# Kernel tuning notes

Hardware: AMD Instinct MI355X
Metric: run time of the kernel (lower is better)

## Reference

```python
import jax, jax.numpy as jnp
import numpy as np

B, S, D = 4, 2048, 768
H, DK, DV = 12, 64, 64
NEG = -1e9
EPS = 1e-5  # torch LayerNorm default


def setup_inputs() -> dict:
    key = jax.random.key(0)
    ks = jax.random.split(key, 12)
    s = 0.02
    return {
        "Q": jax.random.normal(ks[0], (B, S, D), jnp.float32),
        "K": jax.random.normal(ks[1], (B, S, D), jnp.float32),
        "V": jax.random.normal(ks[2], (B, S, D), jnp.float32),
        "attn_pad": jax.random.randint(ks[3], (B, S, S), 0, 2).astype(bool),
        # weights stored [in, out] (transpose of torch Linear layout)
        "Wq": jax.random.normal(ks[4], (D, H * DK), jnp.float32) * s,
        "bq": jnp.zeros((H * DK,), jnp.float32),
        "Wk": jax.random.normal(ks[5], (D, H * DK), jnp.float32) * s,
        "bk": jnp.zeros((H * DK,), jnp.float32),
        "Wv": jax.random.normal(ks[6], (D, H * DV), jnp.float32) * s,
        "bv": jnp.zeros((H * DV,), jnp.float32),
        "Wo": jax.random.normal(ks[7], (H * DV, D), jnp.float32) * s,
        "bo": jnp.zeros((D,), jnp.float32),
        "ln_g": jnp.ones((D,), jnp.float32),
        "ln_b": jnp.zeros((D,), jnp.float32),
    }


def reference(Q, K, V, attn_pad, Wq, bq, Wk, bk, Wv, bv, Wo, bo, ln_g, ln_b):
    residual = Q
    # projections -> [B, H, S, d]
    q = (Q @ Wq + bq).reshape(B, S, H, DK).transpose(0, 2, 1, 3)
    k = (K @ Wk + bk).reshape(B, S, H, DK).transpose(0, 2, 1, 3)
    v = (V @ Wv + bv).reshape(B, S, H, DV).transpose(0, 2, 1, 3)
    # scaled dot-product attention with pad masking
    scores = jnp.einsum("bhqd,bhkd->bhqk", q, k) / np.sqrt(DK).astype(np.float32)
    scores = jnp.where(attn_pad[:, None, :, :], NEG, scores)
    attn = jax.nn.softmax(scores, axis=-1)
    context = jnp.einsum("bhqk,bhkd->bhqd", attn, v)
    context = context.transpose(0, 2, 1, 3).reshape(B, S, H * DV)
    out = context @ Wo + bo + residual
    # LayerNorm over last dim
    mu = jnp.mean(out, axis=-1, keepdims=True)
    var = jnp.mean(jnp.square(out - mu), axis=-1, keepdims=True)
    out = (out - mu) * jax.lax.rsqrt(var + EPS) * ln_g + ln_b
    return out, attn
```

## Files before the change

### kernel.cpp

```cpp
#include <hip/hip_runtime.h>
#include <hip/hip_bf16.h>

#define BB 4
#define SS 2048
#define DD 768
#define HH 12
#define DKV 64
#define NEGBIG (-1e30f)

__global__ __launch_bounds__(256) void proj_gemm(
    const float* __restrict__ X, const float* __restrict__ W,
    const float* __restrict__ bias, float* __restrict__ outp)
{
  const int K = DD, N = DD;
  const int row0 = blockIdx.x * 64;
  const int h    = blockIdx.y;
  const int col0 = h << 6;
  const int tid = threadIdx.x;
  const int ty = tid >> 4, tx = tid & 15;

  __shared__ __align__(16) float As[16 * 64];
  __shared__ __align__(16) float Bs[16 * 64];

  float acc[4][4] = {};
  for (int k0 = 0; k0 < K; k0 += 16) {
    {
      int r = tid >> 2, c = (tid & 3) << 2;
      float4 a4 = *(const float4*)&X[(size_t)(row0 + r) * K + k0 + c];
      As[(c + 0) * 64 + r] = a4.x; As[(c + 1) * 64 + r] = a4.y;
      As[(c + 2) * 64 + r] = a4.z; As[(c + 3) * 64 + r] = a4.w;
    }
    {
      int r = tid >> 4, c = (tid & 15) << 2;
      *(float4*)&Bs[r * 64 + c] = *(const float4*)&W[(size_t)(k0 + r) * N + col0 + c];
    }
    __syncthreads();
#pragma unroll
    for (int kk = 0; kk < 16; ++kk) {
      float4 a4 = *(float4*)&As[kk * 64 + ty * 4];
      float4 b4 = *(float4*)&Bs[kk * 64 + tx * 4];
      float a[4] = {a4.x, a4.y, a4.z, a4.w};
      float b[4] = {b4.x, b4.y, b4.z, b4.w};
#pragma unroll
      for (int i = 0; i < 4; i++)
#pragma unroll
        for (int j = 0; j < 4; j++) acc[i][j] += a[i] * b[j];
    }
    __syncthreads();
  }
  float4 bv4 = *(const float4*)&bias[col0 + tx * 4];
#pragma unroll
  for (int i = 0; i < 4; i++) {
    int row = row0 + ty * 4 + i;
    int b = row >> 11, s = row & (SS - 1);
    float4 o;
    o.x = acc[i][0] + bv4.x; o.y = acc[i][1] + bv4.y;
    o.z = acc[i][2] + bv4.z; o.w = acc[i][3] + bv4.w;
    *(float4*)&outp[(((size_t)b * HH + h) * SS + s) * DKV + tx * 4] = o;
  }
}

__global__ __launch_bounds__(256) void outproj_gemm(
    const float* __restrict__ X, const float* __restrict__ W,
    const float* __restrict__ bias, const float* __restrict__ resid,
    float* __restrict__ outp)
{
  const int K = DD, N = DD;
  const int row0 = blockIdx.x * 64;
  const int col0 = blockIdx.y << 6;
  const int tid = threadIdx.x;
  const int ty = tid >> 4, tx = tid & 15;

  __shared__ __align__(16) float As[16 * 64];
  __shared__ __align__(16) float Bs[16 * 64];

  float acc[4][4] = {};
  for (int k0 = 0; k0 < K; k0 += 16) {
    {
      int r = tid >> 2, c = (tid & 3) << 2;
      float4 a4 = *(const float4*)&X[(size_t)(row0 + r) * K + k0 + c];
      As[(c + 0) * 64 + r] = a4.x; As[(c + 1) * 64 + r] = a4.y;
      As[(c + 2) * 64 + r] = a4.z; As[(c + 3) * 64 + r] = a4.w;
    }
    {
      int r = tid >> 4, c = (tid & 15) << 2;
      *(float4*)&Bs[r * 64 + c] = *(const float4*)&W[(size_t)(k0 + r) * N + col0 + c];
    }
    __syncthreads();
#pragma unroll
    for (int kk = 0; kk < 16; ++kk) {
      float4 a4 = *(float4*)&As[kk * 64 + ty * 4];
      float4 b4 = *(float4*)&Bs[kk * 64 + tx * 4];
      float a[4] = {a4.x, a4.y, a4.z, a4.w};
      float b[4] = {b4.x, b4.y, b4.z, b4.w};
#pragma unroll
      for (int i = 0; i < 4; i++)
#pragma unroll
        for (int j = 0; j < 4; j++) acc[i][j] += a[i] * b[j];
    }
    __syncthreads();
  }
  float4 bv4 = *(const float4*)&bias[col0 + tx * 4];
#pragma unroll
  for (int i = 0; i < 4; i++) {
    int row = row0 + ty * 4 + i;
    float4 r4 = *(const float4*)&resid[(size_t)row * DD + col0 + tx * 4];
    float4 o;
    o.x = acc[i][0] + bv4.x + r4.x; o.y = acc[i][1] + bv4.y + r4.y;
    o.z = acc[i][2] + bv4.z + r4.z; o.w = acc[i][3] + bv4.w + r4.w;
    *(float4*)&outp[(size_t)row * DD + col0 + tx * 4] = o;
  }
}

__global__ __launch_bounds__(256) void attn_kernel(
    const float* __restrict__ qh, const float* __restrict__ kh,
    const float* __restrict__ vh, const int* __restrict__ pad,
    float* __restrict__ attn, float* __restrict__ ctx)
{
  const int qt = blockIdx.x, h = blockIdx.y, b = blockIdx.z;
  const int tid = threadIdx.x;
  const int ty = tid >> 4, tx = tid & 15;

  const float* qbase = qh + (((size_t)b * HH + h) * SS + qt * 64) * DKV;
  const float* kbase = kh + (((size_t)b * HH + h) * SS) * DKV;
  const float* vbase = vh + (((size_t)b * HH + h) * SS) * DKV;

  __shared__ __align__(16) float QsT[64 * 64];
  __shared__ __align__(16) float KV[64 * 64];
  __shared__ __align__(16) float Sc[64 * 68];
  __shared__ float red[64 * 4];
  __shared__ float mrow[64], lrow[64], mnew_s[64];

  {
    int r = tid >> 2, cb = (tid & 3) << 4;
    const float* qr = qbase + (size_t)r * DKV;
#pragma unroll
    for (int q = 0; q < 4; q++) {
      float4 v = *(const float4*)(qr + cb + q * 4);
      QsT[(cb + q * 4 + 0) * 64 + r] = v.x; QsT[(cb + q * 4 + 1) * 64 + r] = v.y;
      QsT[(cb + q * 4 + 2) * 64 + r] = v.z; QsT[(cb + q * 4 + 3) * 64 + r] = v.w;
    }
  }
  if (tid < 64) { mrow[tid] = NEGBIG; lrow[tid] = 0.f; }
  __syncthreads();

  for (int kc = 0; kc < SS / 64; ++kc) {
    int kc0 = kc << 6;
    {
      int r = tid >> 2, cb = (tid & 3) << 4;
      const float* krow = kbase + (size_t)(kc0 + r) * DKV;
#pragma unroll
      for (int q = 0; q < 4; q++) {
        float4 v = *(const float4*)(krow + cb + q * 4);
        KV[(cb + q * 4 + 0) * 64 + r] = v.x; KV[(cb + q * 4 + 1) * 64 + r] = v.y;
        KV[(cb + q * 4 + 2) * 64 + r] = v.z; KV[(cb + q * 4 + 3) * 64 + r] = v.w;
      }
    }
    __syncthreads();
    float s[4][4] = {};
#pragma unroll 16
    for (int kk = 0; kk < 64; ++kk) {
      float4 a4 = *(float4*)&QsT[kk * 64 + ty * 4];
      float4 b4 = *(float4*)&KV[kk * 64 + tx * 4];
      float a[4] = {a4.x, a4.y, a4.z, a4.w};
      float bb[4] = {b4.x, b4.y, b4.z, b4.w};
#pragma unroll
      for (int i = 0; i < 4; i++)
#pragma unroll
        for (int j = 0; j < 4; j++) s[i][j] += a[i] * bb[j];
    }
#pragma unroll
    for (int i = 0; i < 4; i++) {
      int qglob = qt * 64 + ty * 4 + i;
      const int4 pm = *(const int4*)&pad[((size_t)b * SS + qglob) * SS + kc0 + tx * 4];
      float4 o;
      o.x = pm.x ? -1e9f : s[i][0] * 0.125f;
      o.y = pm.y ? -1e9f : s[i][1] * 0.125f;
      o.z = pm.z ? -1e9f : s[i][2] * 0.125f;
      o.w = pm.w ? -1e9f : s[i][3] * 0.125f;
      *(float4*)&Sc[(ty * 4 + i) * 68 + tx * 4] = o;
    }
    __syncthreads();
    {
      int r = tid >> 2, seg = tid & 3;
      const float* srow = &Sc[r * 68 + seg * 16];
      float mx = NEGBIG;
#pragma unroll
      for (int t = 0; t < 16; t++) mx = fmaxf(mx, srow[t]);
      red[r * 4 + seg] = mx;
      __syncthreads();
      if (seg == 0) {
        float cm = fmaxf(fmaxf(red[r * 4], red[r * 4 + 1]),
                         fmaxf(red[r * 4 + 2], red[r * 4 + 3]));
        mnew_s[r] = fmaxf(mrow[r], cm);
      }
      __syncthreads();
      float mn = mnew_s[r];
      float se = 0.f;
#pragma unroll
      for (int t = 0; t < 16; t++) se += __expf(srow[t] - mn);
      red[r * 4 + seg] = se;
      __syncthreads();
      if (seg == 0) {
        float ssum = red[r * 4] + red[r * 4 + 1] + red[r * 4 + 2] + red[r * 4 + 3];
        lrow[r] = lrow[r] * __expf(mrow[r] - mn) + ssum;
        mrow[r] = mn;
      }
    }
    __syncthreads();
  }

  float mloc[4], linv[4];
#pragma unroll
  for (int i = 0; i < 4; i++) {
    mloc[i] = mrow[ty * 4 + i];
    linv[i] = 1.f / lrow[ty * 4 + i];
  }
  float cacc[4][4] = {};

  for (int kc = 0; kc < SS / 64; ++kc) {
    int kc0 = kc << 6;
    {
      int r = tid >> 2, cb = (tid & 3) << 4;
      const float* krow = kbase + (size_t)(kc0 + r) * DKV;
#pragma unroll
      for (int q = 0; q < 4; q++) {
        float4 v = *(const float4*)(krow + cb + q * 4);
        KV[(cb + q * 4 + 0) * 64 + r] = v.x; KV[(cb + q * 4 + 1) * 64 + r] = v.y;
        KV[(cb + q * 4 + 2) * 64 + r] = v.z; KV[(cb + q * 4 + 3) * 64 + r] = v.w;
      }
    }
    __syncthreads();
    float s[4][4] = {};
#pragma unroll 16
    for (int kk = 0; kk < 64; ++kk) {
      float4 a4 = *(float4*)&QsT[kk * 64 + ty * 4];
      float4 b4 = *(float4*)&KV[kk * 64 + tx * 4];
      float a[4] = {a4.x, a4.y, a4.z, a4.w};
      float bb[4] = {b4.x, b4.y, b4.z, b4.w};
#pragma unroll
      for (int i = 0; i < 4; i++)
#pragma unroll
        for (int j = 0; j < 4; j++) s[i][j] += a[i] * bb[j];
    }
#pragma unroll
    for (int i = 0; i < 4; i++) {
      int qglob = qt * 64 + ty * 4 + i;
      const int4 pm = *(const int4*)&pad[((size_t)b * SS + qglob) * SS + kc0 + tx * 4];
      float sv0 = pm.x ? -1e9f : s[i][0] * 0.125f;
      float sv1 = pm.y ? -1e9f : s[i][1] * 0.125f;
      float sv2 = pm.z ? -1e9f : s[i][2] * 0.125f;
      float sv3 = pm.w ? -1e9f : s[i][3] * 0.125f;
      float4 o;
      o.x = __expf(sv0 - mloc[i]) * linv[i];
      o.y = __expf(sv1 - mloc[i]) * linv[i];
      o.z = __expf(sv2 - mloc[i]) * linv[i];
      o.w = __expf(sv3 - mloc[i]) * linv[i];
      *(float4*)&attn[(((size_t)b * HH + h) * SS + qglob) * SS + kc0 + tx * 4] = o;
      *(float4*)&Sc[(ty * 4 + i) * 68 + tx * 4] = o;
    }
    __syncthreads();
    {
      int r = tid >> 2, cb = (tid & 3) << 4;
      const float* vrow = vbase + (size_t)(kc0 + r) * DKV;
#pragma unroll
      for (int q = 0; q < 4; q++)
        *(float4*)&KV[r * 64 + cb + q * 4] = *(const float4*)(vrow + cb + q * 4);
    }
    __syncthreads();
#pragma unroll 8
    for (int kk = 0; kk < 64; ++kk) {
      float a0 = Sc[(ty * 4 + 0) * 68 + kk];
      float a1 = Sc[(ty * 4 + 1) * 68 + kk];
      float a2 = Sc[(ty * 4 + 2) * 68 + kk];
      float a3 = Sc[(ty * 4 + 3) * 68 + kk];
      float4 b4 = *(float4*)&KV[kk * 64 + tx * 4];
      float bb[4] = {b4.x, b4.y, b4.z, b4.w};
#pragma unroll
      for (int j = 0; j < 4; j++) {
        cacc[0][j] += a0 * bb[j];
        cacc[1][j] += a1 * bb[j];
        cacc[2][j] += a2 * bb[j];
        cacc[3][j] += a3 * bb[j];
      }
    }
    __syncthreads();
  }
#pragma unroll
  for (int i = 0; i < 4; i++) {
    int row = qt * 64 + ty * 4 + i;
    float4 o = {cacc[i][0], cacc[i][1], cacc[i][2], cacc[i][3]};
    *(float4*)&ctx[((size_t)b * SS + row) * DD + h * DKV + tx * 4] = o;
  }
}

__global__ __launch_bounds__(256) void ln_kernel(
    const float* __restrict__ x, const float* __restrict__ gam,
    const float* __restrict__ bet, float* __restrict__ out)
{
  const int row = blockIdx.x;
  const int tid = threadIdx.x;
  const float* xr = x + (size_t)row * DD;
  float v0 = xr[tid], v1 = xr[tid + 256], v2 = xr[tid + 512];
  float s1 = v0 + v1 + v2;
  float s2 = v0 * v0 + v1 * v1 + v2 * v2;
  __shared__ float r1[256], r2[256];
  r1[tid] = s1; r2[tid] = s2;
  __syncthreads();
  for (int off = 128; off > 0; off >>= 1) {
    if (tid < off) { r1[tid] += r1[tid + off]; r2[tid] += r2[tid + off]; }
    __syncthreads();
  }
  __shared__ float mu_s, rs_s;
  if (tid == 0) {
    float mu = r1[0] * (1.f / 768.f);
    float var = r2[0] * (1.f / 768.f) - mu * mu;
    mu_s = mu; rs_s = rsqrtf(var + 1e-5f);
  }
  __syncthreads();
  float mu = mu_s, rs = rs_s;
  float* orow = out + (size_t)row * DD;
  orow[tid]       = (v0 - mu) * rs * gam[tid]       + bet[tid];
  orow[tid + 256] = (v1 - mu) * rs * gam[tid + 256] + bet[tid + 256];
  orow[tid + 512] = (v2 - mu) * rs * gam[tid + 512] + bet[tid + 512];
}

extern "C" void kernel_launch(void* const* d_in, const int* in_sizes, int n_in,
                              void* d_out, int out_size, void* d_ws, size_t ws_size,
                              hipStream_t stream) {
  const float* Q   = (const float*)d_in[0];
  const float* K   = (const float*)d_in[1];
  const float* V   = (const float*)d_in[2];
  const int*   pad = (const int*)d_in[3];
  const float* Wq  = (const float*)d_in[4];
  const float* bq  = (const float*)d_in[5];
  const float* Wk  = (const float*)d_in[6];
  const float* bk  = (const float*)d_in[7];
  const float* Wv  = (const float*)d_in[8];
  const float* bv  = (const float*)d_in[9];
  const float* Wo  = (const float*)d_in[10];
  const float* bo  = (const float*)d_in[11];
  const float* lng = (const float*)d_in[12];
  const float* lnb = (const float*)d_in[13];

  float* out  = (float*)d_out;
  float* attn = out + (size_t)BB * SS * DD;

  const size_t NQ = (size_t)BB * SS * DD;
  float* ws  = (float*)d_ws;
  float* qh  = ws;
  float* khp = ws + NQ;
  float* vhp = ws + 2 * NQ;
  float* ctx = ws + 3 * NQ;
  float* tmp = qh;

  dim3 gproj(SS * BB / 64, DD / 64);
  proj_gemm<<<gproj, 256, 0, stream>>>(Q, Wq, bq, qh);
  proj_gemm<<<gproj, 256, 0, stream>>>(K, Wk, bk, khp);
  proj_gemm<<<gproj, 256, 0, stream>>>(V, Wv, bv, vhp);

  dim3 gattn(SS / 64, HH, BB);
  attn_kernel<<<gattn, 256, 0, stream>>>(qh, khp, vhp, pad, attn, ctx);

  outproj_gemm<<<gproj, 256, 0, stream>>>(ctx, Wo, bo, Q, tmp);

  ln_kernel<<<BB * SS, 256, 0, stream>>>(tmp, lng, lnb, out);
}
```

Baseline: 2.435 ms.

## Rewrite attention kernel with bf16 MFMA and register-resident online softmax

Replaces the scalar fp32 attention kernel with one that converts Q, K and V tiles to bf16 in XOR-swizzled shared memory and computes QK^T and PV with 16x16x32 bf16 MFMA instructions. Row max and sum for the softmax are now reduced with wave shuffles in registers instead of shared-memory reductions and extra barriers. It targets the compute-bound fp32 FMA loops and sync overhead, at the cost of bf16 precision in scores and context. The attention-matrix writes and pad reads become scalar strided per-lane accesses instead of float4, which may hurt memory efficiency.

Result: faster. 1.966 ms (-19.3%).

```diff
diff --git a/kernel.cpp b/kernel.cpp
--- a/kernel.cpp
+++ b/kernel.cpp
@@ -1,5 +1,4 @@
 #include <hip/hip_runtime.h>
-#include <hip/hip_bf16.h>
 
 #define BB 4
 #define SS 2048
@@ -7,6 +6,16 @@
 #define HH 12
 #define DKV 64
 #define NEGBIG (-1e30f)
+
+typedef float f32x4 __attribute__((ext_vector_type(4)));
+typedef short bf16x8 __attribute__((ext_vector_type(8)));
+typedef short s16x4 __attribute__((ext_vector_type(4)));
+
+__device__ inline unsigned short f2bf(float f) {
+  unsigned u = __builtin_bit_cast(unsigned, f);
+  u += 0x7fffu + ((u >> 16) & 1u);
+  return (unsigned short)(u >> 16);
+}
 
 __global__ __launch_bounds__(256) void proj_gemm(
     const float* __restrict__ X, const float* __restrict__ W,
@@ -112,185 +121,179 @@
   }
 }
 
-__global__ __launch_bounds__(256) void attn_kernel(
+__device__ inline bf16x8 ldfrag(const short* base, int row, int bytecol) {
+  int off = row * 128 + (bytecol ^ ((row & 7) << 4));
+  return *(const bf16x8*)((const char*)base + off);
+}
+
+__device__ inline void stage_rows64(const float* __restrict__ src, short* dst, int tid) {
+#pragma unroll
+  for (int j = 0; j < 4; ++j) {
+    int li = j * 256 + tid;
+    int row = li >> 4;
+    int c4 = (li & 15) << 2;
+    f32x4 v = *(const f32x4*)(src + row * 64 + c4);
+    s16x4 o;
+    o[0] = (short)f2bf(v[0]); o[1] = (short)f2bf(v[1]);
+    o[2] = (short)f2bf(v[2]); o[3] = (short)f2bf(v[3]);
+    int off = row * 128 + (((c4) << 1) ^ ((row & 7) << 4));
+    *(s16x4*)((char*)dst + off) = o;
+  }
+}
+
+__device__ inline void stage_vt(const float* __restrict__ vsrc, short* dst, int tid) {
+  int kb = tid >> 4;
+  int db = tid & 15;
+  const float* p0 = vsrc + (size_t)(4 * kb) * 64 + 4 * db;
+  f32x4 r0 = *(const f32x4*)(p0);
+  f32x4 r1 = *(const f32x4*)(p0 + 64);
+  f32x4 r2 = *(const f32x4*)(p0 + 128);
+  f32x4 r3 = *(const f32x4*)(p0 + 192);
+#pragma unroll
+  for (int i = 0; i < 4; ++i) {
+    s16x4 o;
+    o[0] = (short)f2bf(r0[i]); o[1] = (short)f2bf(r1[i]);
+    o[2] = (short)f2bf(r2[i]); o[3] = (short)f2bf(r3[i]);
+    int row = 4 * db + i;
+    int off = row * 128 + ((kb * 8) ^ ((row & 7) << 4));
+    *(s16x4*)((char*)dst + off) = o;
+  }
+}
+
+__global__ __launch_bounds__(256) void attn_mfma(
     const float* __restrict__ qh, const float* __restrict__ kh,
     const float* __restrict__ vh, const int* __restrict__ pad,
     float* __restrict__ attn, float* __restrict__ ctx)
 {
   const int qt = blockIdx.x, h = blockIdx.y, b = blockIdx.z;
   const int tid = threadIdx.x;
-  const int ty = tid >> 4, tx = tid & 15;
-
-  const float* qbase = qh + (((size_t)b * HH + h) * SS + qt * 64) * DKV;
+  const int lane = tid & 63, w = tid >> 6;
+  const int c = lane & 15, g = lane >> 4;
+
+  __shared__ __align__(16) short Qs[64 * 64];
+  __shared__ __align__(16) short KsS[64 * 64];
+  __shared__ __align__(16) short VtS[64 * 64];
+  __shared__ __align__(16) short PsS[64 * 64];
+
+  const float* qbase = qh + (((size_t)b * HH + h) * SS + (size_t)qt * 64) * DKV;
   const float* kbase = kh + (((size_t)b * HH + h) * SS) * DKV;
   const float* vbase = vh + (((size_t)b * HH + h) * SS) * DKV;
 
-  __shared__ __align__(16) float QsT[64 * 64];
-  __shared__ __align__(16) float KV[64 * 64];
-  __shared__ __align__(16) float Sc[64 * 68];
-  __shared__ float red[64 * 4];
-  __shared__ float mrow[64], lrow[64], mnew_s[64];
-
-  {
-    int r = tid >> 2, cb = (tid & 3) << 4;
-    const float* qr = qbase + (size_t)r * DKV;
-#pragma unroll
-    for (int q = 0; q < 4; q++) {
-      float4 v = *(const float4*)(qr + cb + q * 4);
-      QsT[(cb + q * 4 + 0) * 64 + r] = v.x; QsT[(cb + q * 4 + 1) * 64 + r] = v.y;
-      QsT[(cb + q * 4 + 2) * 64 + r] = v.z; QsT[(cb + q * 4 + 3) * 64 + r] = v.w;
-    }
-  }
-  if (tid < 64) { mrow[tid] = NEGBIG; lrow[tid] = 0.f; }
+  stage_rows64(qbase, Qs, tid);
   __syncthreads();
 
+  const bf16x8 aq0 = ldfrag(Qs, 16 * w + c, g * 16);
+  const bf16x8 aq1 = ldfrag(Qs, 16 * w + c, 64 + g * 16);
+
+  const int q0 = qt * 64 + 16 * w;
+
+  float mrun[4] = {NEGBIG, NEGBIG, NEGBIG, NEGBIG};
+  float lrun[4] = {0.f, 0.f, 0.f, 0.f};
+
   for (int kc = 0; kc < SS / 64; ++kc) {
-    int kc0 = kc << 6;
-    {
-      int r = tid >> 2, cb = (tid & 3) << 4;
-      const float* krow = kbase + (size_t)(kc0 + r) * DKV;
-#pragma unroll
-      for (int q = 0; q < 4; q++) {
-        float4 v = *(const float4*)(krow + cb + q * 4);
-        KV[(cb + q * 4 + 0) * 64 + r] = v.x; KV[(cb + q * 4 + 1) * 64 + r] = v.y;
-        KV[(cb + q * 4 + 2) * 64 + r] = v.z; KV[(cb + q * 4 + 3) * 64 + r] = v.w;
+    const int kc0 = kc << 6;
+    __syncthreads();
+    stage_rows64(kbase + (size_t)kc0 * DKV, KsS, tid);
+    __syncthreads();
+
+    f32x4 accS[4] = {{0.f,0.f,0.f,0.f},{0.f,0.f,0.f,0.f},{0.f,0.f,0.f,0.f},{0.f,0.f,0.f,0.f}};
+#pragma unroll
+    for (int nt = 0; nt < 4; ++nt) {
+      bf16x8 b0 = ldfrag(KsS, 16 * nt + c, g * 16);
+      bf16x8 b1 = ldfrag(KsS, 16 * nt + c, 64 + g * 16);
+      accS[nt] = __builtin_amdgcn_mfma_f32_16x16x32_bf16(aq0, b0, accS[nt], 0, 0, 0);
+      accS[nt] = __builtin_amdgcn_mfma_f32_16x16x32_bf16(aq1, b1, accS[nt], 0, 0, 0);
+    }
+
+    float sc[4][4];
+    float cmax[4] = {NEGBIG, NEGBIG, NEGBIG, NEGBIG};
+#pragma unroll
+    for (int r = 0; r < 4; ++r) {
+      const int* prow = pad + ((size_t)b * SS + (q0 + 4 * g + r)) * SS + kc0 + c;
+#pragma unroll
+      for (int nt = 0; nt < 4; ++nt) {
+        float s = accS[nt][r] * 0.125f;
+        s = prow[16 * nt] ? -1e9f : s;
+        sc[r][nt] = s;
+        cmax[r] = fmaxf(cmax[r], s);
       }
     }
-    __syncthreads();
-    float s[4][4] = {};
-#pragma unroll 16
-    for (int kk = 0; kk < 64; ++kk) {
-      float4 a4 = *(float4*)&QsT[kk * 64 + ty * 4];
-      float4 b4 = *(float4*)&KV[kk * 64 + tx * 4];
-      float a[4] = {a4.x, a4.y, a4.z, a4.w};
-      float bb[4] = {b4.x, b4.y, b4.z, b4.w};
-#pragma unroll
-      for (int i = 0; i < 4; i++)
-#pragma unroll
-        for (int j = 0; j < 4; j++) s[i][j] += a[i] * bb[j];
-    }
-#pragma unroll
-    for (int i = 0; i < 4; i++) {
-      int qglob = qt * 64 + ty * 4 + i;
-      const int4 pm = *(const int4*)&pad[((size_t)b * SS + qglob) * SS + kc0 + tx * 4];
-      float4 o;
-      o.x = pm.x ? -1e9f : s[i][0] * 0.125f;
-      o.y = pm.y ? -1e9f : s[i][1] * 0.125f;
-      o.z = pm.z ? -1e9f : s[i][2] * 0.125f;
-      o.w = pm.w ? -1e9f : s[i][3] * 0.125f;
-      *(float4*)&Sc[(ty * 4 + i) * 68 + tx * 4] = o;
-    }
-    __syncthreads();
-    {
-      int r = tid >> 2, seg = tid & 3;
-      const float* srow = &Sc[r * 68 + seg * 16];
-      float mx = NEGBIG;
-#pragma unroll
-      for (int t = 0; t < 16; t++) mx = fmaxf(mx, srow[t]);
-      red[r * 4 + seg] = mx;
-      __syncthreads();
-      if (seg == 0) {
-        float cm = fmaxf(fmaxf(red[r * 4], red[r * 4 + 1]),
-                         fmaxf(red[r * 4 + 2], red[r * 4 + 3]));
-        mnew_s[r] = fmaxf(mrow[r], cm);
+#pragma unroll
+    for (int r = 0; r < 4; ++r) {
+#pragma unroll
+      for (int m = 1; m <= 8; m <<= 1)
+        cmax[r] = fmaxf(cmax[r], __shfl_xor(cmax[r], m));
+      float mn = fmaxf(mrun[r], cmax[r]);
+      float corr = __expf(mrun[r] - mn);
+      float ps = 0.f;
+#pragma unroll
+      for (int nt = 0; nt < 4; ++nt) ps += __expf(sc[r][nt] - mn);
+#pragma unroll
+      for (int m = 1; m <= 8; m <<= 1) ps += __shfl_xor(ps, m);
+      lrun[r] = lrun[r] * corr + ps;
+      mrun[r] = mn;
+    }
+  }
+
+  float linv[4];
+#pragma unroll
+  for (int r = 0; r < 4; ++r) linv[r] = 1.f / lrun[r];
+
+  f32x4 cacc[4] = {{0.f,0.f,0.f,0.f},{0.f,0.f,0.f,0.f},{0.f,0.f,0.f,0.f},{0.f,0.f,0.f,0.f}};
+  float* attb = attn + ((size_t)b * HH + h) * SS * SS;
+
+  for (int kc = 0; kc < SS / 64; ++kc) {
+    const int kc0 = kc << 6;
+    __syncthreads();
+    stage_rows64(kbase + (size_t)kc0 * DKV, KsS, tid);
+    stage_vt(vbase + (size_t)kc0 * DKV, VtS, tid);
+    __syncthreads();
+
+    f32x4 accS[4] = {{0.f,0.f,0.f,0.f},{0.f,0.f,0.f,0.f},{0.f,0.f,0.f,0.f},{0.f,0.f,0.f,0.f}};
+#pragma unroll
+    for (int nt = 0; nt < 4; ++nt) {
+      bf16x8 b0 = ldfrag(KsS, 16 * nt + c, g * 16);
+      bf16x8 b1 = ldfrag(KsS, 16 * nt + c, 64 + g * 16);
+      accS[nt] = __builtin_amdgcn_mfma_f32_16x16x32_bf16(aq0, b0, accS[nt], 0, 0, 0);
+      accS[nt] = __builtin_amdgcn_mfma_f32_16x16x32_bf16(aq1, b1, accS[nt], 0, 0, 0);
+    }
+
+#pragma unroll
+    for (int r = 0; r < 4; ++r) {
+      const int q = q0 + 4 * g + r;
+      const int* prow = pad + ((size_t)b * SS + q) * SS + kc0 + c;
+      float* arow = attb + (size_t)q * SS + kc0 + c;
+      const int psrow = 4 * g + r;
+#pragma unroll
+      for (int nt = 0; nt < 4; ++nt) {
+        float s = accS[nt][r] * 0.125f;
+        s = prow[16 * nt] ? -1e9f : s;
+        float p = __expf(s - mrun[r]) * linv[r];
+        arow[16 * nt] = p;
+        int off = w * 2048 + psrow * 128 + ((((16 * nt + c) << 1)) ^ ((psrow & 7) << 4));
+        *(short*)((char*)PsS + off) = (short)f2bf(p);
       }
-      __syncthreads();
-      float mn = mnew_s[r];
-      float se = 0.f;
-#pragma unroll
-      for (int t = 0; t < 16; t++) se += __expf(srow[t] - mn);
-      red[r * 4 + seg] = se;
-      __syncthreads();
-      if (seg == 0) {
-        float ssum = red[r * 4] + red[r * 4 + 1] + red[r * 4 + 2] + red[r * 4 + 3];
-        lrow[r] = lrow[r] * __expf(mrow[r] - mn) + ssum;
-        mrow[r] = mn;
-      }
-    }
-    __syncthreads();
-  }
-
-  float mloc[4], linv[4];
-#pragma unroll
-  for (int i = 0; i < 4; i++) {
-    mloc[i] = mrow[ty * 4 + i];
-    linv[i] = 1.f / lrow[ty * 4 + i];
-  }
-  float cacc[4][4] = {};
-
-  for (int kc = 0; kc < SS / 64; ++kc) {
-    int kc0 = kc << 6;
-    {
-      int r = tid >> 2, cb = (tid & 3) << 4;
-      const float* krow = kbase + (size_t)(kc0 + r) * DKV;
-#pragma unroll
-      for (int q = 0; q < 4; q++) {
-        float4 v = *(const float4*)(krow + cb + q * 4);
-        KV[(cb + q * 4 + 0) * 64 + r] = v.x; KV[(cb + q * 4 + 1) * 64 + r] = v.y;
-        KV[(cb + q * 4 + 2) * 64 + r] = v.z; KV[(cb + q * 4 + 3) * 64 + r] = v.w;
-      }
-    }
-    __syncthreads();
-    float s[4][4] = {};
-#pragma unroll 16
-    for (int kk = 0; kk < 64; ++kk) {
-      float4 a4 = *(float4*)&QsT[kk * 64 + ty * 4];
-      float4 b4 = *(float4*)&KV[kk * 64 + tx * 4];
-      float a[4] = {a4.x, a4.y, a4.z, a4.w};
-      float bb[4] = {b4.x, b4.y, b4.z, b4.w};
-#pragma unroll
-      for (int i = 0; i < 4; i++)
-#pragma unroll
-        for (int j = 0; j < 4; j++) s[i][j] += a[i] * bb[j];
-    }
-#pragma unroll
-    for (int i = 0; i < 4; i++) {
-      int qglob = qt * 64 + ty * 4 + i;
-      const int4 pm = *(const int4*)&pad[((size_t)b * SS + qglob) * SS + kc0 + tx * 4];
-      float sv0 = pm.x ? -1e9f : s[i][0] * 0.125f;
-      float sv1 = pm.y ? -1e9f : s[i][1] * 0.125f;
-      float sv2 = pm.z ? -1e9f : s[i][2] * 0.125f;
-      float sv3 = pm.w ? -1e9f : s[i][3] * 0.125f;
-      float4 o;
-      o.x = __expf(sv0 - mloc[i]) * linv[i];
-      o.y = __expf(sv1 - mloc[i]) * linv[i];
-      o.z = __expf(sv2 - mloc[i]) * linv[i];
-      o.w = __expf(sv3 - mloc[i]) * linv[i];
-      *(float4*)&attn[(((size_t)b * HH + h) * SS + qglob) * SS + kc0 + tx * 4] = o;
-      *(float4*)&Sc[(ty * 4 + i) * 68 + tx * 4] = o;
-    }
-    __syncthreads();
-    {
-      int r = tid >> 2, cb = (tid & 3) << 4;
-      const float* vrow = vbase + (size_t)(kc0 + r) * DKV;
-#pragma unroll
-      for (int q = 0; q < 4; q++)
-        *(float4*)&KV[r * 64 + cb + q * 4] = *(const float4*)(vrow + cb + q * 4);
-    }
-    __syncthreads();
-#pragma unroll 8
-    for (int kk = 0; kk < 64; ++kk) {
-      float a0 = Sc[(ty * 4 + 0) * 68 + kk];
-      float a1 = Sc[(ty * 4 + 1) * 68 + kk];
-      float a2 = Sc[(ty * 4 + 2) * 68 + kk];
-      float a3 = Sc[(ty * 4 + 3) * 68 + kk];
-      float4 b4 = *(float4*)&KV[kk * 64 + tx * 4];
-      float bb[4] = {b4.x, b4.y, b4.z, b4.w};
-#pragma unroll
-      for (int j = 0; j < 4; j++) {
-        cacc[0][j] += a0 * bb[j];
-        cacc[1][j] += a1 * bb[j];
-        cacc[2][j] += a2 * bb[j];
-        cacc[3][j] += a3 * bb[j];
-      }
-    }
-    __syncthreads();
-  }
-#pragma unroll
-  for (int i = 0; i < 4; i++) {
-    int row = qt * 64 + ty * 4 + i;
-    float4 o = {cacc[i][0], cacc[i][1], cacc[i][2], cacc[i][3]};
-    *(float4*)&ctx[((size_t)b * SS + row) * DD + h * DKV + tx * 4] = o;
+    }
+    asm volatile("s_waitcnt lgkmcnt(0)" ::: "memory");
+    __builtin_amdgcn_sched_barrier(0);
+
+    const bf16x8 pa0 = *(const bf16x8*)((const char*)PsS + w * 2048 + c * 128 + ((g * 16) ^ ((c & 7) << 4)));
+    const bf16x8 pa1 = *(const bf16x8*)((const char*)PsS + w * 2048 + c * 128 + ((64 + g * 16) ^ ((c & 7) << 4)));
+#pragma unroll
+    for (int nt = 0; nt < 4; ++nt) {
+      bf16x8 v0 = ldfrag(VtS, 16 * nt + c, g * 16);
+      bf16x8 v1 = ldfrag(VtS, 16 * nt + c, 64 + g * 16);
+      cacc[nt] = __builtin_amdgcn_mfma_f32_16x16x32_bf16(pa0, v0, cacc[nt], 0, 0, 0);
+      cacc[nt] = __builtin_amdgcn_mfma_f32_16x16x32_bf16(pa1, v1, cacc[nt], 0, 0, 0);
+    }
+  }
+
+#pragma unroll
+  for (int r = 0; r < 4; ++r) {
+    int row = q0 + 4 * g + r;
+    float* crow = ctx + ((size_t)b * SS + row) * DD + h * DKV + c;
+#pragma unroll
+    for (int nt = 0; nt < 4; ++nt) crow[16 * nt] = cacc[nt][r];
   }
 }
 
@@ -360,7 +363,7 @@
   proj_gemm<<<gproj, 256, 0, stream>>>(V, Wv, bv, vhp);
 
   dim3 gattn(SS / 64, HH, BB);
-  attn_kernel<<<gattn, 256, 0, stream>>>(qh, khp, vhp, pad, attn, ctx);
+  attn_mfma<<<gattn, 256, 0, stream>>>(qh, khp, vhp, pad, attn, ctx);
 
   outproj_gemm<<<gproj, 256, 0, stream>>>(ctx, Wo, bo, Q, tmp);
 
```
